# Kernel optimization log

Measured on AMD Instinct MI355X. Metric: run time of the kernel, lower is better.

The kernel has to match this reference:

```python
import jax, jax.numpy as jnp
import numpy as np

CURV_BOUNDS = (-2.0, 2.0)
THRESH = 0.01   # |k| below this -> Euclidean branch
EPS = 1e-5

B, S, D = 4, 2048, 512


def setup_inputs() -> dict:
    key = jax.random.key(0)
    ks = jax.random.split(key, 8)
    x = jax.random.normal(ks[0], (B, S, D), jnp.float32)
    sc = 1.0 / np.sqrt(D)  # ~ nn.Linear default init scale
    Wq = jax.random.uniform(ks[1], (D, D), jnp.float32, -sc, sc)
    bq = jax.random.uniform(ks[2], (D,), jnp.float32, -sc, sc)
    Wk = jax.random.uniform(ks[3], (D, D), jnp.float32, -sc, sc)
    bk = jax.random.uniform(ks[4], (D,), jnp.float32, -sc, sc)
    Wv = jax.random.uniform(ks[5], (D, D), jnp.float32, -sc, sc)
    bv = jax.random.uniform(ks[6], (D,), jnp.float32, -sc, sc)
    curvature_raw = jnp.float32(0.5)   # init_curvature
    temperature = jnp.float32(1.0)
    mask = jnp.triu(jnp.ones((S, S), dtype=bool), 1)  # causal: True = masked out
    return {"x": x, "Wq": Wq, "bq": bq, "Wk": Wk, "bk": bk, "Wv": Wv,
            "bv": bv, "curvature_raw": curvature_raw,
            "temperature": temperature, "mask": mask}


def _curvature(raw):
    k_min, k_max = CURV_BOUNDS
    return k_min + (k_max - k_min) * (jnp.tanh(raw) + 1.0) / 2.0


def _project(u, k):
    # project_to_manifold: identity (euclid), Poincare-ball clip (k<0), sphere renorm (k>0)
    n = jnp.sqrt(jnp.sum(u * u, axis=-1, keepdims=True) + 1e-12)
    absk = jnp.abs(k)
    sk = jnp.sqrt(jnp.maximum(absk, EPS))
    max_norm = (1.0 - 1e-3) / sk                      # ball radius 1/sqrt(|k|)
    u_hyp = u * jnp.minimum(1.0, max_norm / n)
    u_sph = u / (n * sk)                              # sphere radius 1/sqrt(k)
    return jnp.where(absk < THRESH, u, jnp.where(k < 0, u_hyp, u_sph))


def reference(x, Wq, bq, Wk, bk, Wv, bv, curvature_raw, temperature, mask):
    k = _curvature(curvature_raw)
    q = x @ Wq.T + bq
    kk = x @ Wk.T + bk
    v = x @ Wv.T + bv
    qm = _project(q, k)
    km = _project(kk, k)

    # pairwise quantities without materializing [B,S,S,D]
    dots = jnp.einsum('bid,bjd->bij', qm, km)         # [B,S,S]
    qn2 = jnp.sum(qm * qm, axis=-1)                   # [B,S]
    kn2 = jnp.sum(km * km, axis=-1)                   # [B,S]
    diff2 = jnp.maximum(qn2[:, :, None] + kn2[:, None, :] - 2.0 * dots, 0.0)

    absk = jnp.abs(k)
    sk = jnp.sqrt(jnp.maximum(absk, EPS))

    d_euc = jnp.sqrt(diff2 + 1e-12)
    # hyperbolic (Poincare ball, c=|k|): acosh(1 + 2c|x-y|^2 / ((1-c|x|^2)(1-c|y|^2))) / sqrt(c)
    denom = jnp.maximum((1.0 - absk * qn2)[:, :, None] * (1.0 - absk * kn2)[:, None, :], EPS)
    arg = 1.0 + 2.0 * absk * diff2 / denom
    d_hyp = jnp.arccosh(jnp.maximum(arg, 1.0 + 1e-7)) / sk
    # spherical (radius 1/sqrt(k)): arccos(k * <x,y>) / sqrt(k)
    cosang = jnp.clip(absk * dots, -1.0 + 1e-7, 1.0 - 1e-7)
    d_sph = jnp.arccos(cosang) / sk

    dist = jnp.where(absk < THRESH, d_euc, jnp.where(k < 0, d_hyp, d_sph))

    scores = -dist / (temperature + 1e-8)
    scores = jnp.where(mask[None, :, :], -jnp.inf, scores)
    attention = jax.nn.softmax(scores, axis=-1)       # [B,S,S]
    output = jnp.einsum('bij,bjd->bid', attention, v) # [B,S,D]
    return output, attention
```

## Files before the change

kernel.cpp:

```cpp
#include <hip/hip_runtime.h>
#include <hip/hip_bf16.h>
#include <math.h>

typedef unsigned short u16;
typedef float float4e __attribute__((ext_vector_type(4)));
typedef short short8 __attribute__((ext_vector_type(8)));
typedef unsigned short ushort8 __attribute__((ext_vector_type(8)));
typedef unsigned short u16x4 __attribute__((ext_vector_type(4)));

#define SEQ 2048
#define DIM 512
#define NB  4

__device__ __forceinline__ float bf2f(u16 h) {
    return __uint_as_float(((unsigned)h) << 16);
}
__device__ __forceinline__ u16 f2bf(float f) {
    __hip_bfloat16 h = __float2bfloat16(f);
    return *reinterpret_cast<u16*>(&h);
}
__device__ __forceinline__ float curv_of(float raw) {
    return -2.0f + 2.0f * (tanhf(raw) + 1.0f);
}
__device__ __forceinline__ void gl_lds16(const u16* g, u16* lds) {
    __builtin_amdgcn_global_load_lds(
        (const __attribute__((address_space(1))) unsigned int*)g,
        (__attribute__((address_space(3))) unsigned int*)lds, 16, 0, 0);
}

__global__ __launch_bounds__(256) void cvt_all_kernel(
    const float* __restrict__ x, const float* __restrict__ Wq,
    const float* __restrict__ Wk, const float* __restrict__ Wv,
    u16* __restrict__ x_bf, u16* __restrict__ Wcat, float* __restrict__ lsum)
{
    const int n_x = NB * SEQ * DIM, n_w = DIM * DIM;
    int gid = blockIdx.x * 256 + threadIdx.x;
    if (gid < NB * SEQ) lsum[gid] = 0.f;
    int i4 = gid * 4;
    if (i4 < n_x) {
        float4 v = *(const float4*)&x[i4];
        u16x4 h = {f2bf(v.x), f2bf(v.y), f2bf(v.z), f2bf(v.w)};
        *(u16x4*)&x_bf[i4] = h;
    } else if (i4 < n_x + 3 * n_w) {
        int j = i4 - n_x;
        const float* W = (j < n_w) ? Wq : (j < 2 * n_w ? Wk : Wv);
        int off = j % n_w;
        float4 v = *(const float4*)&W[off];
        u16x4 h = {f2bf(v.x), f2bf(v.y), f2bf(v.z), f2bf(v.w)};
        *(u16x4*)&Wcat[j] = h;
    }
}

__global__ __launch_bounds__(256, 2) void gemm_qkv_kernel(
    const u16* __restrict__ A, const u16* __restrict__ Bt,
    u16* __restrict__ C, u16* __restrict__ vT,
    const float* __restrict__ bq, const float* __restrict__ bk, const float* __restrict__ bv)
{
    const int lda = 512, ldb = 512, ldc = 1536;
    int bn = blockIdx.x, bm = blockIdx.y;

    __shared__ __align__(16) u16 As[128 * 64];
    __shared__ __align__(16) u16 Bs[128 * 64];

    int t = threadIdx.x, wave = t >> 6, lane = t & 63;
    int wr = wave >> 1, wc = wave & 1;
    int lrow = lane & 15, quad = lane >> 4;
    int srow = lane >> 3, sc8 = lane & 7;

    const u16* Ab = A + (size_t)(bm * 128) * lda;
    const u16* Bb = Bt + (size_t)(bn * 128) * ldb;

    float4e acc[4][4];
#pragma unroll
    for (int i = 0; i < 4; i++)
#pragma unroll
        for (int j = 0; j < 4; j++) acc[i][j] = (float4e){0.f, 0.f, 0.f, 0.f};

    for (int kt = 0; kt < 8; ++kt) {
        int k0 = kt << 6;
        __syncthreads();
#pragma unroll
        for (int h = 0; h < 4; ++h) {
            int q = wave * 4 + h;
            int row = q * 8 + srow;
            int c = sc8 ^ (row & 7);
            gl_lds16(Ab + (size_t)row * lda + k0 + c * 8, &As[q * 512]);
            gl_lds16(Bb + (size_t)row * ldb + k0 + c * 8, &Bs[q * 512]);
        }
        __syncthreads();
#pragma unroll
        for (int kk = 0; kk < 2; ++kk) {
            short8 af[4], bfr[4];
#pragma unroll
            for (int im = 0; im < 4; im++) {
                int R = wr * 64 + im * 16 + lrow;
                af[im] = *(const short8*)&As[R * 64 + (((kk * 4 + quad) ^ (R & 7)) * 8)];
            }
#pragma unroll
            for (int in = 0; in < 4; in++) {
                int R = wc * 64 + in * 16 + lrow;
                bfr[in] = *(const short8*)&Bs[R * 64 + (((kk * 4 + quad) ^ (R & 7)) * 8)];
            }
#pragma unroll
            for (int im = 0; im < 4; im++)
#pragma unroll
                for (int in = 0; in < 4; in++)
                    acc[im][in] = __builtin_amdgcn_mfma_f32_16x16x32_bf16(af[im], bfr[in], acc[im][in], 0, 0, 0);
        }
    }

#pragma unroll
    for (int in = 0; in < 4; in++) {
        int gj = bn * 128 + wc * 64 + in * 16 + lrow;
        float bias = (gj < 512) ? bq[gj] : (gj < 1024 ? bk[gj - 512] : bv[gj - 1024]);
#pragma unroll
        for (int im = 0; im < 4; im++) {
            int gi0 = bm * 128 + wr * 64 + im * 16 + quad * 4;
            u16x4 pack;
#pragma unroll
            for (int r = 0; r < 4; r++) {
                u16 hv = f2bf(acc[im][in][r] + bias);
                C[(size_t)(gi0 + r) * ldc + gj] = hv;
                pack[r] = hv;
            }
            if (gj >= 1024) {
                int bb = gi0 >> 11, s = gi0 & 2047;
                *(u16x4*)&vT[((size_t)bb * DIM + (gj - 1024)) * SEQ + s] = pack;
            }
        }
    }
}

__global__ __launch_bounds__(256, 4) void gemm_scores_kernel(
    const u16* __restrict__ qm, const u16* __restrict__ km,
    u16* __restrict__ attnH,
    float* __restrict__ lsum,
    const float* __restrict__ qn2v, const float* __restrict__ kn2v,
    const float* __restrict__ curvp, const float* __restrict__ tempp)
{
    const int lda = 512, ldb = 512, ldc = SEQ;
    int bn = blockIdx.x, bm = blockIdx.y, b = blockIdx.z;
    if (bn > 2 * bm + 1) return;

    __shared__ __align__(16) u16 As[128 * 64];
    __shared__ __align__(16) u16 Bs[64 * 64];

    int t = threadIdx.x, wave = t >> 6, lane = t & 63;
    int wr = wave >> 1, wc = wave & 1;
    int lrow = lane & 15, quad = lane >> 4;
    int srow = lane >> 3, sc8 = lane & 7;

    const u16* Ab = qm + (size_t)b * SEQ * DIM + (size_t)(bm * 128) * lda;
    const u16* Bb = km + (size_t)b * SEQ * DIM + (size_t)(bn * 64) * ldb;

    float4e acc[4][2];
#pragma unroll
    for (int i = 0; i < 4; i++)
#pragma unroll
        for (int j = 0; j < 2; j++) acc[i][j] = (float4e){0.f, 0.f, 0.f, 0.f};

    for (int kt = 0; kt < 8; ++kt) {
        int k0 = kt << 6;
        __syncthreads();
#pragma unroll
        for (int h = 0; h < 4; ++h) {
            int q = wave * 4 + h;
            int row = q * 8 + srow;
            int c = sc8 ^ (row & 7);
            gl_lds16(Ab + (size_t)row * lda + k0 + c * 8, &As[q * 512]);
        }
#pragma unroll
        for (int h = 0; h < 2; ++h) {
            int q = wave * 2 + h;
            int row = q * 8 + srow;
            int c = sc8 ^ (row & 7);
            gl_lds16(Bb + (size_t)row * ldb + k0 + c * 8, &Bs[q * 512]);
        }
        __syncthreads();
#pragma unroll
        for (int kk = 0; kk < 2; ++kk) {
            short8 af[4], bfr[2];
#pragma unroll
            for (int im = 0; im < 4; im++) {
                int R = wr * 64 + im * 16 + lrow;
                af[im] = *(const short8*)&As[R * 64 + (((kk * 4 + quad) ^ (R & 7)) * 8)];
            }
#pragma unroll
            for (int in = 0; in < 2; in++) {
                int R = wc * 32 + in * 16 + lrow;
                bfr[in] = *(const short8*)&Bs[R * 64 + (((kk * 4 + quad) ^ (R & 7)) * 8)];
            }
#pragma unroll
            for (int im = 0; im < 4; im++)
#pragma unroll
                for (int in = 0; in < 2; in++)
                    acc[im][in] = __builtin_amdgcn_mfma_f32_16x16x32_bf16(af[im], bfr[in], acc[im][in], 0, 0, 0);
        }
    }

    float kv = curv_of(curvp[0]);
    float absk = fabsf(kv);
    float sk = sqrtf(fmaxf(absk, 1e-5f));
    float invT = 1.0f / (tempp[0] + 1e-8f);
    float Cexp = -1.4426950408889634f * invT;
    u16* Cb = attnH + (size_t)b * SEQ * SEQ;

    float psum[4][4];
#pragma unroll
    for (int im = 0; im < 4; im++)
#pragma unroll
        for (int r = 0; r < 4; r++) psum[im][r] = 0.f;

    float kn[2];
#pragma unroll
    for (int in = 0; in < 2; in++)
        kn[in] = kn2v[b * SEQ + bn * 64 + wc * 32 + in * 16 + lrow];

#pragma unroll
    for (int im = 0; im < 4; im++) {
#pragma unroll
        for (int r = 0; r < 4; r++) {
            int gi = bm * 128 + wr * 64 + im * 16 + quad * 4 + r;
            float qn = qn2v[b * SEQ + gi];
#pragma unroll
            for (int in = 0; in < 2; in++) {
                int gj = bn * 64 + wc * 32 + in * 16 + lrow;
                float dot = acc[im][in][r];
                float diff2 = fmaxf(qn + kn[in] - 2.f * dot, 0.f);
                float dist;
                if (absk < 0.01f) {
                    dist = sqrtf(diff2 + 1e-12f);
                } else if (kv < 0.f) {
                    float denom = fmaxf((1.f - absk * qn) * (1.f - absk * kn[in]), 1e-5f);
                    float arg = fmaxf(1.f + 2.f * absk * diff2 / denom, 1.f + 1e-7f);
                    dist = acoshf(arg) / sk;
                } else {
                    float c = fminf(fmaxf(absk * dot, -1.f + 1e-7f), 1.f - 1e-7f);
                    dist = acosf(c) / sk;
                }
                float e = (gj <= gi) ? exp2f(dist * Cexp) : 0.f;
                Cb[(size_t)gi * ldc + gj] = f2bf(e);
                psum[im][r] += e;
            }
        }
    }
#pragma unroll
    for (int im = 0; im < 4; im++)
#pragma unroll
        for (int r = 0; r < 4; r++) {
            float v = psum[im][r];
            v += __shfl_xor(v, 1);
            v += __shfl_xor(v, 2);
            v += __shfl_xor(v, 4);
            v += __shfl_xor(v, 8);
            if (lrow == 0) {
                int gi = bm * 128 + wr * 64 + im * 16 + quad * 4 + r;
                atomicAdd(&lsum[b * SEQ + gi], v);
            }
        }
}

__global__ __launch_bounds__(256, 8) void gemm_pv_kernel(
    const u16* __restrict__ attnH, const u16* __restrict__ vT,
    float* __restrict__ out, const float* __restrict__ lsum)
{
    const int lda = SEQ, ldb = SEQ, ldc = DIM;
    int bn = blockIdx.x, bm = blockIdx.y, b = blockIdx.z;

    __shared__ __align__(16) u16 As[64 * 64];
    __shared__ __align__(16) u16 Bs[64 * 64];

    int t = threadIdx.x, wave = t >> 6, lane = t & 63;
    int wr = wave >> 1, wc = wave & 1;
    int lrow = lane & 15, quad = lane >> 4;
    int srow = lane >> 3, sc = lane & 7;

    const u16* Ab = attnH + (size_t)b * SEQ * SEQ + (size_t)(bm * 64) * lda;
    const u16* Bb = vT + (size_t)b * DIM * SEQ + (size_t)(bn * 64) * ldb;

    float4e acc[2][2];
#pragma unroll
    for (int i = 0; i < 2; i++)
#pragma unroll
        for (int j = 0; j < 2; j++) acc[i][j] = (float4e){0.f, 0.f, 0.f, 0.f};

    for (int kt = 0; kt <= bm; ++kt) {
        int k0 = kt << 6;
        __syncthreads();
#pragma unroll
        for (int h = 0; h < 2; ++h) {
            int q = wave * 2 + h;
            int row = q * 8 + srow;
            int c = sc ^ (row & 7);
            gl_lds16(Ab + (size_t)row * lda + k0 + c * 8, &As[q * 512]);
            gl_lds16(Bb + (size_t)row * ldb + k0 + c * 8, &Bs[q * 512]);
        }
        __syncthreads();
#pragma unroll
        for (int s = 0; s < 2; ++s) {
            short8 af[2], bfr[2];
#pragma unroll
            for (int im = 0; im < 2; im++) {
                int R = wr * 32 + im * 16 + lrow;
                af[im] = *(const short8*)&As[R * 64 + (((s * 4 + quad) ^ (R & 7)) * 8)];
            }
#pragma unroll
            for (int in = 0; in < 2; in++) {
                int R = wc * 32 + in * 16 + lrow;
                bfr[in] = *(const short8*)&Bs[R * 64 + (((s * 4 + quad) ^ (R & 7)) * 8)];
            }
#pragma unroll
            for (int im = 0; im < 2; im++)
#pragma unroll
                for (int in = 0; in < 2; in++)
                    acc[im][in] = __builtin_amdgcn_mfma_f32_16x16x32_bf16(af[im], bfr[in], acc[im][in], 0, 0, 0);
        }
    }

    float* Cb = out + (size_t)b * SEQ * DIM;
#pragma unroll
    for (int im = 0; im < 2; im++)
#pragma unroll
        for (int r = 0; r < 4; r++) {
            int gi = bm * 64 + wr * 32 + im * 16 + quad * 4 + r;
            float invl = 1.0f / lsum[b * SEQ + gi];
#pragma unroll
            for (int in = 0; in < 2; in++) {
                int gd = bn * 64 + wc * 32 + in * 16 + lrow;
                Cb[(size_t)gi * ldc + gd] = acc[im][in][r] * invl;
            }
        }
}

__global__ __launch_bounds__(256) void project_kernel(
    const u16* __restrict__ qkvh,
    u16* __restrict__ qm, u16* __restrict__ km,
    float* __restrict__ qn2, float* __restrict__ kn2,
    const float* __restrict__ curvp)
{
    int wave = threadIdx.x >> 6, lane = threadIdx.x & 63;
    int r = blockIdx.x * 4 + wave;
    float kv = curv_of(curvp[0]);
    float absk = fabsf(kv);
    float sk = sqrtf(fmaxf(absk, 1e-5f));

    const u16* qrow = qkvh + (size_t)r * 1536;
    ushort8 qh = *(const ushort8*)&qrow[lane * 8];
    ushort8 kh = *(const ushort8*)&qrow[512 + lane * 8];

    float qv[8], kw[8];
    float sq = 0.f, s2 = 0.f;
#pragma unroll
    for (int e = 0; e < 8; e++) {
        qv[e] = bf2f(qh[e]); sq += qv[e] * qv[e];
        kw[e] = bf2f(kh[e]); s2 += kw[e] * kw[e];
    }
#pragma unroll
    for (int off = 1; off < 64; off <<= 1) {
        sq += __shfl_xor(sq, off);
        s2 += __shfl_xor(s2, off);
    }

    float sclq, sclk;
    {
        float nq = sqrtf(sq + 1e-12f);
        float nk = sqrtf(s2 + 1e-12f);
        if (absk < 0.01f) { sclq = 1.f; sclk = 1.f; }
        else if (kv < 0.f) {
            float mx = (1.0f - 1e-3f) / sk;
            sclq = fminf(1.f, mx / nq);
            sclk = fminf(1.f, mx / nk);
        } else {
            sclq = 1.f / (nq * sk);
            sclk = 1.f / (nk * sk);
        }
    }
    if (lane == 0) {
        qn2[r] = sq * sclq * sclq;
        kn2[r] = s2 * sclk * sclk;
    }
    ushort8 qo, ko;
#pragma unroll
    for (int e = 0; e < 8; e++) {
        qo[e] = f2bf(qv[e] * sclq);
        ko[e] = f2bf(kw[e] * sclk);
    }
    *(ushort8*)&qm[(size_t)r * 512 + lane * 8] = qo;
    *(ushort8*)&km[(size_t)r * 512 + lane * 8] = ko;
}

__global__ __launch_bounds__(256) void norm_attn_kernel(
    const u16* __restrict__ attnH, const float* __restrict__ lsum,
    float* __restrict__ attnF)
{
    int i = blockIdx.x, b = blockIdx.y, t = threadIdx.x;
    float inv = 1.0f / lsum[b * SEQ + i];
    const u16* rowh = attnH + ((size_t)b * SEQ + i) * SEQ;
    float* row = attnF + ((size_t)b * SEQ + i) * SEQ;
    int L = i + 1;
    int j0 = t * 8;
    float4 lo, hi;
    if (j0 + 8 <= L) {
        ushort8 h = *(const ushort8*)&rowh[j0];
        lo.x = bf2f(h[0]) * inv; lo.y = bf2f(h[1]) * inv;
        lo.z = bf2f(h[2]) * inv; lo.w = bf2f(h[3]) * inv;
        hi.x = bf2f(h[4]) * inv; hi.y = bf2f(h[5]) * inv;
        hi.z = bf2f(h[6]) * inv; hi.w = bf2f(h[7]) * inv;
    } else {
        float v[8];
#pragma unroll
        for (int e = 0; e < 8; e++)
            v[e] = (j0 + e < L) ? bf2f(rowh[j0 + e]) * inv : 0.f;
        lo = (float4){v[0], v[1], v[2], v[3]};
        hi = (float4){v[4], v[5], v[6], v[7]};
    }
    *(float4*)&row[j0] = lo;
    *(float4*)&row[j0 + 4] = hi;
}

extern "C" void kernel_launch(void* const* d_in, const int* in_sizes, int n_in,
                              void* d_out, int out_size, void* d_ws, size_t ws_size,
                              hipStream_t stream) {
    (void)in_sizes; (void)n_in; (void)out_size; (void)ws_size;

    const float* x    = (const float*)d_in[0];
    const float* Wq   = (const float*)d_in[1];
    const float* bq   = (const float*)d_in[2];
    const float* Wk   = (const float*)d_in[3];
    const float* bk   = (const float*)d_in[4];
    const float* Wv   = (const float*)d_in[5];
    const float* bv   = (const float*)d_in[6];
    const float* curv = (const float*)d_in[7];
    const float* temp = (const float*)d_in[8];

    float* out   = (float*)d_out;
    float* attnF = out + (size_t)NB * SEQ * DIM;

    char* ws = (char*)d_ws;
    u16*   x_bf  = (u16*)(ws + 0);
    u16*   Wcat  = (u16*)(ws + 8388608);
    u16*   qkvh  = (u16*)(ws + 9961472);
    u16*   qm    = (u16*)(ws + 35127296);
    u16*   km    = (u16*)(ws + 43515904);
    u16*   vT    = (u16*)(ws + 51904512);
    float* qn2   = (float*)(ws + 60293120);
    float* kn2   = (float*)(ws + 60325888);
    float* lsum  = (float*)(ws + 60358656);
    u16*   attnH = (u16*)(ws + 0);

    {
        int n_tot = (NB * SEQ * DIM + 3 * DIM * DIM) / 4;
        cvt_all_kernel<<<(n_tot + 255) / 256, 256, 0, stream>>>(x, Wq, Wk, Wv, x_bf, Wcat, lsum);
    }

    gemm_qkv_kernel<<<dim3(1536 / 128, 8192 / 128, 1), 256, 0, stream>>>(
        x_bf, Wcat, qkvh, vT, bq, bk, bv);

    project_kernel<<<NB * SEQ / 4, 256, 0, stream>>>(qkvh, qm, km, qn2, kn2, curv);

    gemm_scores_kernel<<<dim3(SEQ / 64, SEQ / 128, NB), 256, 0, stream>>>(
        qm, km, attnH, lsum, qn2, kn2, curv, temp);

    gemm_pv_kernel<<<dim3(DIM / 64, SEQ / 64, NB), 256, 0, stream>>>(
        attnH, vT, out, lsum);

    norm_attn_kernel<<<dim3(SEQ, NB), 256, 0, stream>>>(attnH, lsum, attnF);
}
```

Before: 239.9 us.

## Double-buffer GEMM LDS tiles and fuse attention normalization into PV kernel

Each of the three GEMM kernels now uses double-buffered LDS, so the next K tile is loaded while the current one is multiplied, and each K step needs one barrier instead of two. The QKV GEMM gets a narrower 64-column N tile, which doubles its grid. The separate norm_attn pass is removed: the PV kernel now writes the normalized fp32 attention for the bf16 tiles it already holds in LDS, split across the column blocks, and zero-fills the masked upper triangle. This avoids re-reading the bf16 attention matrix, at the cost of more LDS per block, lower occupancy bounds, and store-heavy work inside the PV loop.

```diff
diff --git a/kernel.cpp b/kernel.cpp
--- a/kernel.cpp
+++ b/kernel.cpp
@@ -51,7 +51,7 @@
     }
 }
 
-__global__ __launch_bounds__(256, 2) void gemm_qkv_kernel(
+__global__ __launch_bounds__(256, 3) void gemm_qkv_kernel(
     const u16* __restrict__ A, const u16* __restrict__ Bt,
     u16* __restrict__ C, u16* __restrict__ vT,
     const float* __restrict__ bq, const float* __restrict__ bk, const float* __restrict__ bv)
@@ -59,8 +59,8 @@
     const int lda = 512, ldb = 512, ldc = 1536;
     int bn = blockIdx.x, bm = blockIdx.y;
 
-    __shared__ __align__(16) u16 As[128 * 64];
-    __shared__ __align__(16) u16 Bs[128 * 64];
+    __shared__ __align__(16) u16 As[2][128 * 64];
+    __shared__ __align__(16) u16 Bs[2][64 * 64];
 
     int t = threadIdx.x, wave = t >> 6, lane = t & 63;
     int wr = wave >> 1, wc = wave & 1;
@@ -68,50 +68,62 @@
     int srow = lane >> 3, sc8 = lane & 7;
 
     const u16* Ab = A + (size_t)(bm * 128) * lda;
-    const u16* Bb = Bt + (size_t)(bn * 128) * ldb;
-
-    float4e acc[4][4];
-#pragma unroll
-    for (int i = 0; i < 4; i++)
-#pragma unroll
-        for (int j = 0; j < 4; j++) acc[i][j] = (float4e){0.f, 0.f, 0.f, 0.f};
-
-    for (int kt = 0; kt < 8; ++kt) {
+    const u16* Bb = Bt + (size_t)(bn * 64) * ldb;
+
+    auto stage = [&](int buf, int kt) {
         int k0 = kt << 6;
-        __syncthreads();
 #pragma unroll
         for (int h = 0; h < 4; ++h) {
             int q = wave * 4 + h;
             int row = q * 8 + srow;
             int c = sc8 ^ (row & 7);
-            gl_lds16(Ab + (size_t)row * lda + k0 + c * 8, &As[q * 512]);
-            gl_lds16(Bb + (size_t)row * ldb + k0 + c * 8, &Bs[q * 512]);
-        }
-        __syncthreads();
+            gl_lds16(Ab + (size_t)row * lda + k0 + c * 8, &As[buf][q * 512]);
+        }
+#pragma unroll
+        for (int h = 0; h < 2; ++h) {
+            int q = wave * 2 + h;
+            int row = q * 8 + srow;
+            int c = sc8 ^ (row & 7);
+            gl_lds16(Bb + (size_t)row * ldb + k0 + c * 8, &Bs[buf][q * 512]);
+        }
+    };
+
+    float4e acc[4][2];
+#pragma unroll
+    for (int i = 0; i < 4; i++)
+#pragma unroll
+        for (int j = 0; j < 2; j++) acc[i][j] = (float4e){0.f, 0.f, 0.f, 0.f};
+
+    stage(0, 0);
+    __syncthreads();
+    for (int kt = 0; kt < 8; ++kt) {
+        int cur = kt & 1;
+        if (kt + 1 < 8) stage(cur ^ 1, kt + 1);
 #pragma unroll
         for (int kk = 0; kk < 2; ++kk) {
-            short8 af[4], bfr[4];
+            short8 af[4], bfr[2];
 #pragma unroll
             for (int im = 0; im < 4; im++) {
                 int R = wr * 64 + im * 16 + lrow;
-                af[im] = *(const short8*)&As[R * 64 + (((kk * 4 + quad) ^ (R & 7)) * 8)];
-            }
-#pragma unroll
-            for (int in = 0; in < 4; in++) {
-                int R = wc * 64 + in * 16 + lrow;
-                bfr[in] = *(const short8*)&Bs[R * 64 + (((kk * 4 + quad) ^ (R & 7)) * 8)];
+                af[im] = *(const short8*)&As[cur][R * 64 + (((kk * 4 + quad) ^ (R & 7)) * 8)];
+            }
+#pragma unroll
+            for (int in = 0; in < 2; in++) {
+                int R = wc * 32 + in * 16 + lrow;
+                bfr[in] = *(const short8*)&Bs[cur][R * 64 + (((kk * 4 + quad) ^ (R & 7)) * 8)];
             }
 #pragma unroll
             for (int im = 0; im < 4; im++)
 #pragma unroll
-                for (int in = 0; in < 4; in++)
+                for (int in = 0; in < 2; in++)
                     acc[im][in] = __builtin_amdgcn_mfma_f32_16x16x32_bf16(af[im], bfr[in], acc[im][in], 0, 0, 0);
         }
-    }
-
-#pragma unroll
-    for (int in = 0; in < 4; in++) {
-        int gj = bn * 128 + wc * 64 + in * 16 + lrow;
+        __syncthreads();
+    }
+
+#pragma unroll
+    for (int in = 0; in < 2; in++) {
+        int gj = bn * 64 + wc * 32 + in * 16 + lrow;
         float bias = (gj < 512) ? bq[gj] : (gj < 1024 ? bk[gj - 512] : bv[gj - 1024]);
 #pragma unroll
         for (int im = 0; im < 4; im++) {
@@ -131,7 +143,7 @@
     }
 }
 
-__global__ __launch_bounds__(256, 4) void gemm_scores_kernel(
+__global__ __launch_bounds__(256, 3) void gemm_scores_kernel(
     const u16* __restrict__ qm, const u16* __restrict__ km,
     u16* __restrict__ attnH,
     float* __restrict__ lsum,
@@ -142,8 +154,8 @@
     int bn = blockIdx.x, bm = blockIdx.y, b = blockIdx.z;
     if (bn > 2 * bm + 1) return;
 
-    __shared__ __align__(16) u16 As[128 * 64];
-    __shared__ __align__(16) u16 Bs[64 * 64];
+    __shared__ __align__(16) u16 As[2][128 * 64];
+    __shared__ __align__(16) u16 Bs[2][64 * 64];
 
     int t = threadIdx.x, wave = t >> 6, lane = t & 63;
     int wr = wave >> 1, wc = wave & 1;
@@ -153,42 +165,47 @@
     const u16* Ab = qm + (size_t)b * SEQ * DIM + (size_t)(bm * 128) * lda;
     const u16* Bb = km + (size_t)b * SEQ * DIM + (size_t)(bn * 64) * ldb;
 
-    float4e acc[4][2];
-#pragma unroll
-    for (int i = 0; i < 4; i++)
-#pragma unroll
-        for (int j = 0; j < 2; j++) acc[i][j] = (float4e){0.f, 0.f, 0.f, 0.f};
-
-    for (int kt = 0; kt < 8; ++kt) {
+    auto stage = [&](int buf, int kt) {
         int k0 = kt << 6;
-        __syncthreads();
 #pragma unroll
         for (int h = 0; h < 4; ++h) {
             int q = wave * 4 + h;
             int row = q * 8 + srow;
             int c = sc8 ^ (row & 7);
-            gl_lds16(Ab + (size_t)row * lda + k0 + c * 8, &As[q * 512]);
+            gl_lds16(Ab + (size_t)row * lda + k0 + c * 8, &As[buf][q * 512]);
         }
 #pragma unroll
         for (int h = 0; h < 2; ++h) {
             int q = wave * 2 + h;
             int row = q * 8 + srow;
             int c = sc8 ^ (row & 7);
-            gl_lds16(Bb + (size_t)row * ldb + k0 + c * 8, &Bs[q * 512]);
-        }
-        __syncthreads();
+            gl_lds16(Bb + (size_t)row * ldb + k0 + c * 8, &Bs[buf][q * 512]);
+        }
+    };
+
+    float4e acc[4][2];
+#pragma unroll
+    for (int i = 0; i < 4; i++)
+#pragma unroll
+        for (int j = 0; j < 2; j++) acc[i][j] = (float4e){0.f, 0.f, 0.f, 0.f};
+
+    stage(0, 0);
+    __syncthreads();
+    for (int kt = 0; kt < 8; ++kt) {
+        int cur = kt & 1;
+        if (kt + 1 < 8) stage(cur ^ 1, kt + 1);
 #pragma unroll
         for (int kk = 0; kk < 2; ++kk) {
             short8 af[4], bfr[2];
 #pragma unroll
             for (int im = 0; im < 4; im++) {
                 int R = wr * 64 + im * 16 + lrow;
-                af[im] = *(const short8*)&As[R * 64 + (((kk * 4 + quad) ^ (R & 7)) * 8)];
+                af[im] = *(const short8*)&As[cur][R * 64 + (((kk * 4 + quad) ^ (R & 7)) * 8)];
             }
 #pragma unroll
             for (int in = 0; in < 2; in++) {
                 int R = wc * 32 + in * 16 + lrow;
-                bfr[in] = *(const short8*)&Bs[R * 64 + (((kk * 4 + quad) ^ (R & 7)) * 8)];
+                bfr[in] = *(const short8*)&Bs[cur][R * 64 + (((kk * 4 + quad) ^ (R & 7)) * 8)];
             }
 #pragma unroll
             for (int im = 0; im < 4; im++)
@@ -196,6 +213,7 @@
                 for (int in = 0; in < 2; in++)
                     acc[im][in] = __builtin_amdgcn_mfma_f32_16x16x32_bf16(af[im], bfr[in], acc[im][in], 0, 0, 0);
         }
+        __syncthreads();
     }
 
     float kv = curv_of(curvp[0]);
@@ -260,15 +278,16 @@
         }
 }
 
-__global__ __launch_bounds__(256, 8) void gemm_pv_kernel(
+__global__ __launch_bounds__(256, 4) void gemm_pv_kernel(
     const u16* __restrict__ attnH, const u16* __restrict__ vT,
-    float* __restrict__ out, const float* __restrict__ lsum)
+    float* __restrict__ out, float* __restrict__ attnF,
+    const float* __restrict__ lsum)
 {
     const int lda = SEQ, ldb = SEQ, ldc = DIM;
     int bn = blockIdx.x, bm = blockIdx.y, b = blockIdx.z;
 
-    __shared__ __align__(16) u16 As[64 * 64];
-    __shared__ __align__(16) u16 Bs[64 * 64];
+    __shared__ __align__(16) u16 As[2][64 * 64];
+    __shared__ __align__(16) u16 Bs[2][64 * 64];
 
     int t = threadIdx.x, wave = t >> 6, lane = t & 63;
     int wr = wave >> 1, wc = wave & 1;
@@ -277,37 +296,54 @@
 
     const u16* Ab = attnH + (size_t)b * SEQ * SEQ + (size_t)(bm * 64) * lda;
     const u16* Bb = vT + (size_t)b * DIM * SEQ + (size_t)(bn * 64) * ldb;
-
-    float4e acc[2][2];
-#pragma unroll
-    for (int i = 0; i < 2; i++)
-#pragma unroll
-        for (int j = 0; j < 2; j++) acc[i][j] = (float4e){0.f, 0.f, 0.f, 0.f};
-
-    for (int kt = 0; kt <= bm; ++kt) {
+    float* attnFb = attnF + (size_t)b * SEQ * SEQ;
+
+    {
+        int r = t >> 2, c4 = t & 3;
+        float4 z = (float4){0.f, 0.f, 0.f, 0.f};
+        for (int kt = bm + 1; kt < 32; ++kt)
+            if ((kt & 7) == bn) {
+                float* dst = attnFb + (size_t)(bm * 64 + r) * SEQ + kt * 64 + c4 * 16;
+                ((float4*)dst)[0] = z; ((float4*)dst)[1] = z;
+                ((float4*)dst)[2] = z; ((float4*)dst)[3] = z;
+            }
+    }
+
+    auto stage = [&](int buf, int kt) {
         int k0 = kt << 6;
-        __syncthreads();
 #pragma unroll
         for (int h = 0; h < 2; ++h) {
             int q = wave * 2 + h;
             int row = q * 8 + srow;
             int c = sc ^ (row & 7);
-            gl_lds16(Ab + (size_t)row * lda + k0 + c * 8, &As[q * 512]);
-            gl_lds16(Bb + (size_t)row * ldb + k0 + c * 8, &Bs[q * 512]);
-        }
-        __syncthreads();
+            gl_lds16(Ab + (size_t)row * lda + k0 + c * 8, &As[buf][q * 512]);
+            gl_lds16(Bb + (size_t)row * ldb + k0 + c * 8, &Bs[buf][q * 512]);
+        }
+    };
+
+    float4e acc[2][2];
+#pragma unroll
+    for (int i = 0; i < 2; i++)
+#pragma unroll
+        for (int j = 0; j < 2; j++) acc[i][j] = (float4e){0.f, 0.f, 0.f, 0.f};
+
+    stage(0, 0);
+    __syncthreads();
+    for (int kt = 0; kt <= bm; ++kt) {
+        int cur = kt & 1;
+        if (kt < bm) stage(cur ^ 1, kt + 1);
 #pragma unroll
         for (int s = 0; s < 2; ++s) {
             short8 af[2], bfr[2];
 #pragma unroll
             for (int im = 0; im < 2; im++) {
                 int R = wr * 32 + im * 16 + lrow;
-                af[im] = *(const short8*)&As[R * 64 + (((s * 4 + quad) ^ (R & 7)) * 8)];
+                af[im] = *(const short8*)&As[cur][R * 64 + (((s * 4 + quad) ^ (R & 7)) * 8)];
             }
 #pragma unroll
             for (int in = 0; in < 2; in++) {
                 int R = wc * 32 + in * 16 + lrow;
-                bfr[in] = *(const short8*)&Bs[R * 64 + (((s * 4 + quad) ^ (R & 7)) * 8)];
+                bfr[in] = *(const short8*)&Bs[cur][R * 64 + (((s * 4 + quad) ^ (R & 7)) * 8)];
             }
 #pragma unroll
             for (int im = 0; im < 2; im++)
@@ -315,6 +351,23 @@
                 for (int in = 0; in < 2; in++)
                     acc[im][in] = __builtin_amdgcn_mfma_f32_16x16x32_bf16(af[im], bfr[in], acc[im][in], 0, 0, 0);
         }
+        if ((kt & 7) == bn) {
+            int r = t >> 2, c4 = t & 3;
+            int gi = bm * 64 + r;
+            float invl = 1.0f / lsum[b * SEQ + gi];
+            const u16* src = &As[cur][r * 64];
+            int j0 = c4 * 2;
+            ushort8 u0 = *(const ushort8*)&src[(j0 ^ (r & 7)) * 8];
+            ushort8 u1 = *(const ushort8*)&src[((j0 + 1) ^ (r & 7)) * 8];
+            float* dst = attnFb + (size_t)gi * SEQ + kt * 64 + c4 * 16;
+            float4 f0 = {bf2f(u0[0]) * invl, bf2f(u0[1]) * invl, bf2f(u0[2]) * invl, bf2f(u0[3]) * invl};
+            float4 f1 = {bf2f(u0[4]) * invl, bf2f(u0[5]) * invl, bf2f(u0[6]) * invl, bf2f(u0[7]) * invl};
+            float4 f2 = {bf2f(u1[0]) * invl, bf2f(u1[1]) * invl, bf2f(u1[2]) * invl, bf2f(u1[3]) * invl};
+            float4 f3 = {bf2f(u1[4]) * invl, bf2f(u1[5]) * invl, bf2f(u1[6]) * invl, bf2f(u1[7]) * invl};
+            ((float4*)dst)[0] = f0; ((float4*)dst)[1] = f1;
+            ((float4*)dst)[2] = f2; ((float4*)dst)[3] = f3;
+        }
+        __syncthreads();
     }
 
     float* Cb = out + (size_t)b * SEQ * DIM;
@@ -389,35 +442,6 @@
     *(ushort8*)&km[(size_t)r * 512 + lane * 8] = ko;
 }
 
-__global__ __launch_bounds__(256) void norm_attn_kernel(
-    const u16* __restrict__ attnH, const float* __restrict__ lsum,
-    float* __restrict__ attnF)
-{
-    int i = blockIdx.x, b = blockIdx.y, t = threadIdx.x;
-    float inv = 1.0f / lsum[b * SEQ + i];
-    const u16* rowh = attnH + ((size_t)b * SEQ + i) * SEQ;
-    float* row = attnF + ((size_t)b * SEQ + i) * SEQ;
-    int L = i + 1;
-    int j0 = t * 8;
-    float4 lo, hi;
-    if (j0 + 8 <= L) {
-        ushort8 h = *(const ushort8*)&rowh[j0];
-        lo.x = bf2f(h[0]) * inv; lo.y = bf2f(h[1]) * inv;
-        lo.z = bf2f(h[2]) * inv; lo.w = bf2f(h[3]) * inv;
-        hi.x = bf2f(h[4]) * inv; hi.y = bf2f(h[5]) * inv;
-        hi.z = bf2f(h[6]) * inv; hi.w = bf2f(h[7]) * inv;
-    } else {
-        float v[8];
-#pragma unroll
-        for (int e = 0; e < 8; e++)
-            v[e] = (j0 + e < L) ? bf2f(rowh[j0 + e]) * inv : 0.f;
-        lo = (float4){v[0], v[1], v[2], v[3]};
-        hi = (float4){v[4], v[5], v[6], v[7]};
-    }
-    *(float4*)&row[j0] = lo;
-    *(float4*)&row[j0 + 4] = hi;
-}
-
 extern "C" void kernel_launch(void* const* d_in, const int* in_sizes, int n_in,
                               void* d_out, int out_size, void* d_ws, size_t ws_size,
                               hipStream_t stream) {
@@ -453,7 +477,7 @@
         cvt_all_kernel<<<(n_tot + 255) / 256, 256, 0, stream>>>(x, Wq, Wk, Wv, x_bf, Wcat, lsum);
     }
 
-    gemm_qkv_kernel<<<dim3(1536 / 128, 8192 / 128, 1), 256, 0, stream>>>(
+    gemm_qkv_kernel<<<dim3(1536 / 64, 8192 / 128, 1), 256, 0, stream>>>(
         x_bf, Wcat, qkvh, vT, bq, bk, bv);
 
     project_kernel<<<NB * SEQ / 4, 256, 0, stream>>>(qkvh, qm, km, qn2, kn2, curv);
@@ -462,7 +486,5 @@
         qm, km, attnH, lsum, qn2, kn2, curv, temp);
 
     gemm_pv_kernel<<<dim3(DIM / 64, SEQ / 64, NB), 256, 0, stream>>>(
-        attnH, vT, out, lsum);
-
-    norm_attn_kernel<<<dim3(SEQ, NB), 256, 0, stream>>>(attnH, lsum, attnF);
-}
+        attnH, vT, out, attnF, lsum);
+}
```

Result: slower. 251.3 us (+4.7%).

## Drop LDS staging in all GEMMs, load MFMA fragments directly from global

Applied to the files above, without the earlier changes.

Replaces the LDS-staged, barrier-synchronised tile loads in the QKV, scores and PV GEMMs with per-wave direct global loads of MFMA fragments. It also retiles: the QKV GEMM goes to 128x64 blocks and the PV GEMM to 128x64 blocks, with a causal K bound of 2*bm+2 and changed launch bounds. The goal is to remove LDS traffic and __syncthreads stalls. In exchange, data that other waves share is no longer reused in the block and is fetched repeatedly from L2/global, and the row-strided 16-byte loads may coalesce poorly.

```diff
diff --git a/kernel.cpp b/kernel.cpp
--- a/kernel.cpp
+++ b/kernel.cpp
@@ -21,11 +21,6 @@
 }
 __device__ __forceinline__ float curv_of(float raw) {
     return -2.0f + 2.0f * (tanhf(raw) + 1.0f);
-}
-__device__ __forceinline__ void gl_lds16(const u16* g, u16* lds) {
-    __builtin_amdgcn_global_load_lds(
-        (const __attribute__((address_space(1))) unsigned int*)g,
-        (__attribute__((address_space(3))) unsigned int*)lds, 16, 0, 0);
 }
 
 __global__ __launch_bounds__(256) void cvt_all_kernel(
@@ -51,7 +46,7 @@
     }
 }
 
-__global__ __launch_bounds__(256, 2) void gemm_qkv_kernel(
+__global__ __launch_bounds__(256, 4) void gemm_qkv_kernel(
     const u16* __restrict__ A, const u16* __restrict__ Bt,
     u16* __restrict__ C, u16* __restrict__ vT,
     const float* __restrict__ bq, const float* __restrict__ bk, const float* __restrict__ bv)
@@ -59,59 +54,45 @@
     const int lda = 512, ldb = 512, ldc = 1536;
     int bn = blockIdx.x, bm = blockIdx.y;
 
-    __shared__ __align__(16) u16 As[128 * 64];
-    __shared__ __align__(16) u16 Bs[128 * 64];
-
     int t = threadIdx.x, wave = t >> 6, lane = t & 63;
     int wr = wave >> 1, wc = wave & 1;
     int lrow = lane & 15, quad = lane >> 4;
-    int srow = lane >> 3, sc8 = lane & 7;
-
-    const u16* Ab = A + (size_t)(bm * 128) * lda;
-    const u16* Bb = Bt + (size_t)(bn * 128) * ldb;
-
-    float4e acc[4][4];
+
+    const u16* Aw = A + (size_t)(bm * 128 + wr * 64) * lda;
+    const u16* Bw = Bt + (size_t)(bn * 64 + wc * 32) * ldb;
+
+    float4e acc[4][2];
 #pragma unroll
     for (int i = 0; i < 4; i++)
 #pragma unroll
-        for (int j = 0; j < 4; j++) acc[i][j] = (float4e){0.f, 0.f, 0.f, 0.f};
-
+        for (int j = 0; j < 2; j++) acc[i][j] = (float4e){0.f, 0.f, 0.f, 0.f};
+
+#pragma unroll
     for (int kt = 0; kt < 8; ++kt) {
-        int k0 = kt << 6;
-        __syncthreads();
-#pragma unroll
-        for (int h = 0; h < 4; ++h) {
-            int q = wave * 4 + h;
-            int row = q * 8 + srow;
-            int c = sc8 ^ (row & 7);
-            gl_lds16(Ab + (size_t)row * lda + k0 + c * 8, &As[q * 512]);
-            gl_lds16(Bb + (size_t)row * ldb + k0 + c * 8, &Bs[q * 512]);
-        }
-        __syncthreads();
-#pragma unroll
-        for (int kk = 0; kk < 2; ++kk) {
-            short8 af[4], bfr[4];
-#pragma unroll
-            for (int im = 0; im < 4; im++) {
-                int R = wr * 64 + im * 16 + lrow;
-                af[im] = *(const short8*)&As[R * 64 + (((kk * 4 + quad) ^ (R & 7)) * 8)];
-            }
-#pragma unroll
-            for (int in = 0; in < 4; in++) {
-                int R = wc * 64 + in * 16 + lrow;
-                bfr[in] = *(const short8*)&Bs[R * 64 + (((kk * 4 + quad) ^ (R & 7)) * 8)];
-            }
+        int k0 = kt * 64;
+        short8 af[4][2], bfr[2][2];
+#pragma unroll
+        for (int im = 0; im < 4; im++)
+#pragma unroll
+            for (int kk = 0; kk < 2; kk++)
+                af[im][kk] = *(const short8*)&Aw[(size_t)(im * 16 + lrow) * lda + k0 + kk * 32 + quad * 8];
+#pragma unroll
+        for (int in = 0; in < 2; in++)
+#pragma unroll
+            for (int kk = 0; kk < 2; kk++)
+                bfr[in][kk] = *(const short8*)&Bw[(size_t)(in * 16 + lrow) * ldb + k0 + kk * 32 + quad * 8];
+#pragma unroll
+        for (int kk = 0; kk < 2; kk++)
 #pragma unroll
             for (int im = 0; im < 4; im++)
 #pragma unroll
-                for (int in = 0; in < 4; in++)
-                    acc[im][in] = __builtin_amdgcn_mfma_f32_16x16x32_bf16(af[im], bfr[in], acc[im][in], 0, 0, 0);
-        }
-    }
-
-#pragma unroll
-    for (int in = 0; in < 4; in++) {
-        int gj = bn * 128 + wc * 64 + in * 16 + lrow;
+                for (int in = 0; in < 2; in++)
+                    acc[im][in] = __builtin_amdgcn_mfma_f32_16x16x32_bf16(af[im][kk], bfr[in][kk], acc[im][in], 0, 0, 0);
+    }
+
+#pragma unroll
+    for (int in = 0; in < 2; in++) {
+        int gj = bn * 64 + wc * 32 + in * 16 + lrow;
         float bias = (gj < 512) ? bq[gj] : (gj < 1024 ? bk[gj - 512] : bv[gj - 1024]);
 #pragma unroll
         for (int im = 0; im < 4; im++) {
@@ -142,16 +123,12 @@
     int bn = blockIdx.x, bm = blockIdx.y, b = blockIdx.z;
     if (bn > 2 * bm + 1) return;
 
-    __shared__ __align__(16) u16 As[128 * 64];
-    __shared__ __align__(16) u16 Bs[64 * 64];
-
     int t = threadIdx.x, wave = t >> 6, lane = t & 63;
     int wr = wave >> 1, wc = wave & 1;
     int lrow = lane & 15, quad = lane >> 4;
-    int srow = lane >> 3, sc8 = lane & 7;
-
-    const u16* Ab = qm + (size_t)b * SEQ * DIM + (size_t)(bm * 128) * lda;
-    const u16* Bb = km + (size_t)b * SEQ * DIM + (size_t)(bn * 64) * ldb;
+
+    const u16* Aw = qm + (size_t)b * SEQ * DIM + (size_t)(bm * 128 + wr * 64) * lda;
+    const u16* Bw = km + (size_t)b * SEQ * DIM + (size_t)(bn * 64 + wc * 32) * ldb;
 
     float4e acc[4][2];
 #pragma unroll
@@ -159,43 +136,27 @@
 #pragma unroll
         for (int j = 0; j < 2; j++) acc[i][j] = (float4e){0.f, 0.f, 0.f, 0.f};
 
+#pragma unroll
     for (int kt = 0; kt < 8; ++kt) {
-        int k0 = kt << 6;
-        __syncthreads();
-#pragma unroll
-        for (int h = 0; h < 4; ++h) {
-            int q = wave * 4 + h;
-            int row = q * 8 + srow;
-            int c = sc8 ^ (row & 7);
-            gl_lds16(Ab + (size_t)row * lda + k0 + c * 8, &As[q * 512]);
-        }
-#pragma unroll
-        for (int h = 0; h < 2; ++h) {
-            int q = wave * 2 + h;
-            int row = q * 8 + srow;
-            int c = sc8 ^ (row & 7);
-            gl_lds16(Bb + (size_t)row * ldb + k0 + c * 8, &Bs[q * 512]);
-        }
-        __syncthreads();
-#pragma unroll
-        for (int kk = 0; kk < 2; ++kk) {
-            short8 af[4], bfr[2];
-#pragma unroll
-            for (int im = 0; im < 4; im++) {
-                int R = wr * 64 + im * 16 + lrow;
-                af[im] = *(const short8*)&As[R * 64 + (((kk * 4 + quad) ^ (R & 7)) * 8)];
-            }
-#pragma unroll
-            for (int in = 0; in < 2; in++) {
-                int R = wc * 32 + in * 16 + lrow;
-                bfr[in] = *(const short8*)&Bs[R * 64 + (((kk * 4 + quad) ^ (R & 7)) * 8)];
-            }
+        int k0 = kt * 64;
+        short8 af[4][2], bfr[2][2];
+#pragma unroll
+        for (int im = 0; im < 4; im++)
+#pragma unroll
+            for (int kk = 0; kk < 2; kk++)
+                af[im][kk] = *(const short8*)&Aw[(size_t)(im * 16 + lrow) * lda + k0 + kk * 32 + quad * 8];
+#pragma unroll
+        for (int in = 0; in < 2; in++)
+#pragma unroll
+            for (int kk = 0; kk < 2; kk++)
+                bfr[in][kk] = *(const short8*)&Bw[(size_t)(in * 16 + lrow) * ldb + k0 + kk * 32 + quad * 8];
+#pragma unroll
+        for (int kk = 0; kk < 2; kk++)
 #pragma unroll
             for (int im = 0; im < 4; im++)
 #pragma unroll
                 for (int in = 0; in < 2; in++)
-                    acc[im][in] = __builtin_amdgcn_mfma_f32_16x16x32_bf16(af[im], bfr[in], acc[im][in], 0, 0, 0);
-        }
+                    acc[im][in] = __builtin_amdgcn_mfma_f32_16x16x32_bf16(af[im][kk], bfr[in][kk], acc[im][in], 0, 0, 0);
     }
 
     float kv = curv_of(curvp[0]);
@@ -260,69 +221,56 @@
         }
 }
 
-__global__ __launch_bounds__(256, 8) void gemm_pv_kernel(
+__global__ __launch_bounds__(256, 4) void gemm_pv_kernel(
     const u16* __restrict__ attnH, const u16* __restrict__ vT,
     float* __restrict__ out, const float* __restrict__ lsum)
 {
     const int lda = SEQ, ldb = SEQ, ldc = DIM;
     int bn = blockIdx.x, bm = blockIdx.y, b = blockIdx.z;
-
-    __shared__ __align__(16) u16 As[64 * 64];
-    __shared__ __align__(16) u16 Bs[64 * 64];
 
     int t = threadIdx.x, wave = t >> 6, lane = t & 63;
     int wr = wave >> 1, wc = wave & 1;
     int lrow = lane & 15, quad = lane >> 4;
-    int srow = lane >> 3, sc = lane & 7;
-
-    const u16* Ab = attnH + (size_t)b * SEQ * SEQ + (size_t)(bm * 64) * lda;
-    const u16* Bb = vT + (size_t)b * DIM * SEQ + (size_t)(bn * 64) * ldb;
-
-    float4e acc[2][2];
-#pragma unroll
-    for (int i = 0; i < 2; i++)
+
+    const u16* Aw = attnH + (size_t)b * SEQ * SEQ + (size_t)(bm * 128 + wr * 64) * lda;
+    const u16* Bw = vT + (size_t)b * DIM * SEQ + (size_t)(bn * 64 + wc * 32) * ldb;
+
+    float4e acc[4][2];
+#pragma unroll
+    for (int i = 0; i < 4; i++)
 #pragma unroll
         for (int j = 0; j < 2; j++) acc[i][j] = (float4e){0.f, 0.f, 0.f, 0.f};
 
-    for (int kt = 0; kt <= bm; ++kt) {
-        int k0 = kt << 6;
-        __syncthreads();
-#pragma unroll
-        for (int h = 0; h < 2; ++h) {
-            int q = wave * 2 + h;
-            int row = q * 8 + srow;
-            int c = sc ^ (row & 7);
-            gl_lds16(Ab + (size_t)row * lda + k0 + c * 8, &As[q * 512]);
-            gl_lds16(Bb + (size_t)row * ldb + k0 + c * 8, &Bs[q * 512]);
-        }
-        __syncthreads();
-#pragma unroll
-        for (int s = 0; s < 2; ++s) {
-            short8 af[2], bfr[2];
-#pragma unroll
-            for (int im = 0; im < 2; im++) {
-                int R = wr * 32 + im * 16 + lrow;
-                af[im] = *(const short8*)&As[R * 64 + (((s * 4 + quad) ^ (R & 7)) * 8)];
-            }
-#pragma unroll
-            for (int in = 0; in < 2; in++) {
-                int R = wc * 32 + in * 16 + lrow;
-                bfr[in] = *(const short8*)&Bs[R * 64 + (((s * 4 + quad) ^ (R & 7)) * 8)];
-            }
-#pragma unroll
-            for (int im = 0; im < 2; im++)
+    int ktEnd = 2 * bm + 2;
+#pragma unroll 2
+    for (int kt = 0; kt < ktEnd; ++kt) {
+        int k0 = kt * 64;
+        short8 af[4][2], bfr[2][2];
+#pragma unroll
+        for (int im = 0; im < 4; im++)
+#pragma unroll
+            for (int kk = 0; kk < 2; kk++)
+                af[im][kk] = *(const short8*)&Aw[(size_t)(im * 16 + lrow) * lda + k0 + kk * 32 + quad * 8];
+#pragma unroll
+        for (int in = 0; in < 2; in++)
+#pragma unroll
+            for (int kk = 0; kk < 2; kk++)
+                bfr[in][kk] = *(const short8*)&Bw[(size_t)(in * 16 + lrow) * ldb + k0 + kk * 32 + quad * 8];
+#pragma unroll
+        for (int kk = 0; kk < 2; kk++)
+#pragma unroll
+            for (int im = 0; im < 4; im++)
 #pragma unroll
                 for (int in = 0; in < 2; in++)
-                    acc[im][in] = __builtin_amdgcn_mfma_f32_16x16x32_bf16(af[im], bfr[in], acc[im][in], 0, 0, 0);
-        }
+                    acc[im][in] = __builtin_amdgcn_mfma_f32_16x16x32_bf16(af[im][kk], bfr[in][kk], acc[im][in], 0, 0, 0);
     }
 
     float* Cb = out + (size_t)b * SEQ * DIM;
 #pragma unroll
-    for (int im = 0; im < 2; im++)
+    for (int im = 0; im < 4; im++)
 #pragma unroll
         for (int r = 0; r < 4; r++) {
-            int gi = bm * 64 + wr * 32 + im * 16 + quad * 4 + r;
+            int gi = bm * 128 + wr * 64 + im * 16 + quad * 4 + r;
             float invl = 1.0f / lsum[b * SEQ + gi];
 #pragma unroll
             for (int in = 0; in < 2; in++) {
@@ -453,7 +401,7 @@
         cvt_all_kernel<<<(n_tot + 255) / 256, 256, 0, stream>>>(x, Wq, Wk, Wv, x_bf, Wcat, lsum);
     }
 
-    gemm_qkv_kernel<<<dim3(1536 / 128, 8192 / 128, 1), 256, 0, stream>>>(
+    gemm_qkv_kernel<<<dim3(1536 / 64, 8192 / 128, 1), 256, 0, stream>>>(
         x_bf, Wcat, qkvh, vT, bq, bk, bv);
 
     project_kernel<<<NB * SEQ / 4, 256, 0, stream>>>(qkvh, qm, km, qn2, kn2, curv);
@@ -461,7 +409,7 @@
     gemm_scores_kernel<<<dim3(SEQ / 64, SEQ / 128, NB), 256, 0, stream>>>(
         qm, km, attnH, lsum, qn2, kn2, curv, temp);
 
-    gemm_pv_kernel<<<dim3(DIM / 64, SEQ / 64, NB), 256, 0, stream>>>(
+    gemm_pv_kernel<<<dim3(DIM / 64, SEQ / 128, NB), 256, 0, stream>>>(
         attnH, vT, out, lsum);
 
     norm_attn_kernel<<<dim3(SEQ, NB), 256, 0, stream>>>(attnH, lsum, attnF);
```

Result: slower. 424.7 us (+77.0%).
